# Performance work log

Measured on AMD Instinct MI355X. Metric: run time of the kernel, lower is better.

Reference implementation:

```python
import jax, jax.numpy as jnp
import numpy as np

B, OBJ, INP, HID = 8, 128, 64, 256
D = 3 * INP  # concatenated per-object feature dim


def setup_inputs() -> dict:
    key = jax.random.key(0)
    ks = jax.random.split(key, 12)
    s = 0.02
    return {
        "x0": jax.random.normal(ks[0], (B, OBJ, INP), jnp.float32),
        "x1": jax.random.normal(ks[1], (B, OBJ, INP), jnp.float32),
        "x2": jax.random.normal(ks[2], (B, OBJ, INP), jnp.float32),
        # weights stored [in, out] so forward is x @ w + b
        "w_enc": jax.random.normal(ks[3], (2 * D, HID), jnp.float32) * s,
        "b_enc": jnp.zeros((HID,), jnp.float32),
        "w1": jax.random.normal(ks[4], (HID, HID), jnp.float32) * s,
        "b1": jnp.zeros((HID,), jnp.float32),
        "w2": jax.random.normal(ks[5], (HID, HID), jnp.float32) * s,
        "b2": jnp.zeros((HID,), jnp.float32),
        "w3": jax.random.normal(ks[6], (HID, HID), jnp.float32) * s,
        "b3": jnp.zeros((HID,), jnp.float32),
        "wd1": jax.random.normal(ks[7], (HID, HID), jnp.float32) * s,
        "bd1": jnp.zeros((HID,), jnp.float32),
        "wd2": jax.random.normal(ks[8], (HID, INP), jnp.float32) * s,
        "bd2": jnp.zeros((INP,), jnp.float32),
    }


def reference(x0, x1, x2, w_enc, b_enc, w1, b1, w2, b2, w3, b3, wd1, bd1, wd2, bd2):
    x = jnp.concatenate([x0, x1, x2], axis=-1)  # [B, N, D]
    # Fused equivalent of Linear(cat(e1, e2)): split w_enc rows into the part
    # acting on the first-object features and the second-object features, then
    # broadcast-add instead of materializing the [B,N,N,2D] concat tensor.
    ea = jnp.einsum("bnd,dh->bnh", x, w_enc[:D])   # acts on data_e1
    eb = jnp.einsum("bnd,dh->bnh", x, w_enc[D:])   # acts on data_e2
    h = jax.nn.relu(ea[:, :, None, :] + eb[:, None, :, :] + b_enc)  # [B,N,N,H]
    h = jax.nn.relu(h @ w1 + b1)
    h = jax.nn.relu(h @ w2 + b2)
    h = h @ w3 + b3              # fc3 has no activation before the mean
    pooled = h.mean(axis=2)      # [B, N, H]
    out = jax.nn.relu(pooled @ wd1 + bd1) @ wd2 + bd2  # [B, N, INP]
    return out
```

## Files before the change

kernel.cpp:

```cpp
#include <hip/hip_runtime.h>
#include <stdint.h>


#define HID 256
#define NOBJ 128
#define NROW 1024

typedef __attribute__((ext_vector_type(8))) short short8;
typedef __attribute__((ext_vector_type(4))) float float4v;
typedef __attribute__((ext_vector_type(16))) float float16v;
typedef __attribute__((ext_vector_type(2))) unsigned int uint2v;

__device__ __forceinline__ unsigned int f2bf_u(float f) {
    unsigned int u = __builtin_bit_cast(unsigned int, f);
    u += 0x7fffu + ((u >> 16) & 1u);
    return u >> 16;
}
__device__ __forceinline__ unsigned int pack2(float a, float b) {
    return f2bf_u(a) | (f2bf_u(b) << 16);
}
__device__ __forceinline__ float relu(float v) { return v > 0.f ? v : 0.f; }

__device__ __forceinline__ void lds_barrier() {
    asm volatile("s_waitcnt lgkmcnt(0)\n\ts_barrier" ::: "memory");
}

__global__ void setup_kernel(const float* __restrict__ x0, const float* __restrict__ x1,
                             const float* __restrict__ x2, const float* __restrict__ w_enc,
                             const float* __restrict__ b_enc,
                             const float* __restrict__ w1, const float* __restrict__ w2,
                             const float* __restrict__ w3,
                             unsigned short* __restrict__ wt,
                             float* __restrict__ ea, float* __restrict__ eb) {
    const int bx = blockIdx.x, t = threadIdx.x;
    __shared__ float lw[256][33];
    __shared__ float xs[2][192];
    if (bx < 24) {
        const int m = bx >> 3, tau = bx & 7;
        const float* w = (m == 0) ? w1 : (m == 1) ? w2 : w3;
        const int n = t & 31, kk = t >> 5;
#pragma unroll
        for (int rep = 0; rep < 32; ++rep) {
            int k = rep * 8 + kk;
            lw[k][n] = w[k * 256 + tau * 32 + n];
        }
        __syncthreads();
        unsigned short* outp = wt + (m * 8 + tau) * 8192;
        const int lane = t & 63, wq = t >> 6;
        const int h5 = lane >> 5, l31n = lane & 31;
#pragma unroll
        for (int rep = 0; rep < 4; ++rep) {
            const int kb = wq * 4 + rep;
            short8 v;
#pragma unroll
            for (int e = 0; e < 8; ++e)
                v[e] = (short)f2bf_u(lw[kb * 16 + h5 * 8 + e][l31n]);
            *(short8*)(outp + kb * 512 + lane * 8) = v;
        }
        return;
    }
    const int e = bx - 24;
    for (int idx = t; idx < 384; idx += 256) {
        int r = idx / 192, d = idx % 192;
        int row = e * 2 + r;
        float v = (d < 64) ? x0[row * 64 + d]
                : (d < 128) ? x1[row * 64 + d - 64]
                : x2[row * 64 + d - 128];
        xs[r][d] = v;
    }
    __syncthreads();
    float aA[2] = {0.f, 0.f}, aB[2] = {0.f, 0.f};
#pragma unroll 16
    for (int d = 0; d < 192; ++d) {
        float wa = w_enc[d * 256 + t];
        float wb = w_enc[(192 + d) * 256 + t];
#pragma unroll
        for (int r = 0; r < 2; ++r) { aA[r] += xs[r][d] * wa; aB[r] += xs[r][d] * wb; }
    }
    float be = b_enc[t];
#pragma unroll
    for (int r = 0; r < 2; ++r) {
        ea[(e * 2 + r) * 256 + t] = aA[r] + be;
        eb[(e * 2 + r) * 256 + t] = aB[r];
    }
}

__global__ __launch_bounds__(256, 2) void pair_kernel(
        const float* __restrict__ ea, const float* __restrict__ eb,
        const unsigned short* __restrict__ wt,
        const float* __restrict__ b1, const float* __restrict__ b2,
        const float* __restrict__ b3,
        const float* __restrict__ wd1, const float* __restrict__ bd1,
        const float* __restrict__ wd2, const float* __restrict__ bd2,
        float* __restrict__ out) {
    __shared__ __align__(16) unsigned short hbuf[128 * 256];

    const int w = blockIdx.x, b = w >> 7;
    const int t = threadIdx.x, wv = t >> 6, lane = t & 63;
    const int l31 = lane & 31, h5 = lane >> 5;
    const int n0 = wv * 64;

    const unsigned short* aptr = wt + lane * 8;

    short8 af[4][2], bfr[2][4];
#pragma unroll
    for (int pg = 0; pg < 3; ++pg) {
        af[pg][0] = *(const short8*)(aptr + ((wv * 2 + 0) * 16 + pg) * 512);
        af[pg][1] = *(const short8*)(aptr + ((wv * 2 + 1) * 16 + pg) * 512);
    }

    {
        const float4v va = *(const float4v*)(ea + w * 256 + lane * 4);
        const float* ebbase = eb + (b * NOBJ) * 256;
        const int c = lane >> 1, sub = (lane & 1) * 4;
#pragma unroll 4
        for (int jj = 0; jj < 32; ++jj) {
            const int j = wv * 32 + jj;
            float4v vb = *(const float4v*)(ebbase + j * 256 + lane * 4);
            int addr = j * 256 + ((c ^ (j & 31)) << 3) + sub;
            *(uint2v*)(hbuf + addr) = (uint2v){
                pack2(relu(va[0] + vb[0]), relu(va[1] + vb[1])),
                pack2(relu(va[2] + vb[2]), relu(va[3] + vb[3]))};
        }
    }
    lds_barrier();

    int jb[4];
#pragma unroll
    for (int tj = 0; tj < 4; ++tj) jb[tj] = (tj * 32 + l31) * 256;
#pragma unroll
    for (int tj = 0; tj < 4; ++tj)
        bfr[0][tj] = *(const short8*)(hbuf + jb[tj] + ((h5 ^ l31) << 3));

    float16v acc[2][4];

#pragma unroll
    for (int l = 0; l < 3; ++l) {
        const float* bias = (l == 0) ? b1 : (l == 1) ? b2 : b3;
#pragma unroll
        for (int tn = 0; tn < 2; ++tn)
#pragma unroll
            for (int q = 0; q < 4; ++q) {
                float4v bv = *(const float4v*)(bias + n0 + tn * 32 + q * 8 + h5 * 4);
#pragma unroll
                for (int i = 0; i < 4; ++i)
#pragma unroll
                    for (int tj = 0; tj < 4; ++tj)
                        acc[tn][tj][q * 4 + i] = bv[i];
            }
#pragma unroll
        for (int kb = 0; kb < 16; ++kb) {
            const int g = l * 16 + kb, gp = g + 3;
            if (gp < 48) {
                const int lp = gp >> 4, kp = gp & 15;
                af[gp & 3][0] = *(const short8*)(aptr + ((lp * 8 + wv * 2 + 0) * 16 + kp) * 512);
                af[gp & 3][1] = *(const short8*)(aptr + ((lp * 8 + wv * 2 + 1) * 16 + kp) * 512);
            }
            if (kb < 15) {
                const int off = ((((kb + 1) * 2 + h5) ^ l31) << 3);
#pragma unroll
                for (int tj = 0; tj < 4; ++tj)
                    bfr[(kb + 1) & 1][tj] = *(const short8*)(hbuf + jb[tj] + off);
            }
#pragma unroll
            for (int tn = 0; tn < 2; ++tn)
#pragma unroll
                for (int tj = 0; tj < 4; ++tj)
                    acc[tn][tj] = __builtin_amdgcn_mfma_f32_32x32x16_bf16(
                        af[g & 3][tn], bfr[kb & 1][tj], acc[tn][tj], 0, 0, 0);
        }
        lds_barrier();

        if (l < 2) {
#pragma unroll
            for (int tn = 0; tn < 2; ++tn)
#pragma unroll
                for (int q = 0; q < 4; ++q) {
                    const int nb_ = n0 + tn * 32 + 8 * q + 4 * h5;
                    const int cn = nb_ >> 3, sub = nb_ & 7;
#pragma unroll
                    for (int tj = 0; tj < 4; ++tj) {
                        const int j = tj * 32 + l31;
                        int addr = j * 256 + ((cn ^ l31) << 3) + sub;
                        *(uint2v*)(hbuf + addr) = (uint2v){
                            pack2(relu(acc[tn][tj][q * 4]), relu(acc[tn][tj][q * 4 + 1])),
                            pack2(relu(acc[tn][tj][q * 4 + 2]), relu(acc[tn][tj][q * 4 + 3]))};
                    }
                }
            lds_barrier();
#pragma unroll
            for (int tj = 0; tj < 4; ++tj)
                bfr[0][tj] = *(const short8*)(hbuf + jb[tj] + ((h5 ^ l31) << 3));
        }
    }

    float* fs = (float*)hbuf;
    {
#pragma unroll
        for (int tn = 0; tn < 2; ++tn)
#pragma unroll
            for (int r = 0; r < 16; ++r) {
                float s = acc[tn][0][r] + acc[tn][1][r] + acc[tn][2][r] + acc[tn][3][r];
                s += __shfl_xor(s, 1);
                s += __shfl_xor(s, 2);
                s += __shfl_xor(s, 4);
                s += __shfl_xor(s, 8);
                s += __shfl_xor(s, 16);
                if (l31 == 0) {
                    const int n = n0 + tn * 32 + (r & 3) + 8 * (r >> 2) + 4 * h5;
                    fs[n] = s * 0.0078125f;
                }
            }
    }
    __syncthreads();
    {
        float a1 = bd1[t];
#pragma unroll 16
        for (int k = 0; k < 256; ++k) a1 += fs[k] * wd1[k * 256 + t];
        __syncthreads();
        fs[256 + t] = relu(a1);
    }
    __syncthreads();
    {
        const int o = lane;
        float p = 0.f;
        const float* w2p = wd2 + (wv * 64) * 64 + o;
#pragma unroll 16
        for (int kk = 0; kk < 64; ++kk) p += fs[256 + wv * 64 + kk] * w2p[kk * 64];
        fs[512 + wv * 64 + o] = p;
    }
    __syncthreads();
    if (t < 64)
        out[w * 64 + t] = fs[512 + t] + fs[576 + t] + fs[640 + t] + fs[704 + t] + bd2[t];
}

extern "C" void kernel_launch(void* const* d_in, const int* in_sizes, int n_in,
                              void* d_out, int out_size, void* d_ws, size_t ws_size,
                              hipStream_t stream) {
    const float* x0    = (const float*)d_in[0];
    const float* x1    = (const float*)d_in[1];
    const float* x2    = (const float*)d_in[2];
    const float* w_enc = (const float*)d_in[3];
    const float* b_enc = (const float*)d_in[4];
    const float* w1    = (const float*)d_in[5];
    const float* b1    = (const float*)d_in[6];
    const float* w2    = (const float*)d_in[7];
    const float* b2    = (const float*)d_in[8];
    const float* w3    = (const float*)d_in[9];
    const float* b3    = (const float*)d_in[10];
    const float* wd1   = (const float*)d_in[11];
    const float* bd1   = (const float*)d_in[12];
    const float* wd2   = (const float*)d_in[13];
    const float* bd2   = (const float*)d_in[14];
    float* out = (float*)d_out;

    unsigned short* wt = (unsigned short*)d_ws;
    float* ea = (float*)((char*)d_ws + 3 * 65536 * sizeof(unsigned short));
    float* eb = ea + NROW * HID;

    setup_kernel<<<536, 256, 0, stream>>>(x0, x1, x2, w_enc, b_enc, w1, w2, w3, wt, ea, eb);
    pair_kernel<<<NROW, 256, 0, stream>>>(ea, eb, wt, b1, b2, b3,
                                          wd1, bd1, wd2, bd2, out);
}
```

Before: 169.7 us.

## Store activation tile in MFMA fragment-major LDS layout instead of XOR swizzle

```diff
diff --git a/kernel.cpp b/kernel.cpp
--- a/kernel.cpp
+++ b/kernel.cpp
@@ -10,6 +10,7 @@
 typedef __attribute__((ext_vector_type(4))) float float4v;
 typedef __attribute__((ext_vector_type(16))) float float16v;
 typedef __attribute__((ext_vector_type(2))) unsigned int uint2v;
+typedef __attribute__((ext_vector_type(4))) unsigned int uint4v;
 
 __device__ __forceinline__ unsigned int f2bf_u(float f) {
     unsigned int u = __builtin_bit_cast(unsigned int, f);
@@ -110,27 +111,38 @@
     }
 
     {
-        const float4v va = *(const float4v*)(ea + w * 256 + lane * 4);
         const float* ebbase = eb + (b * NOBJ) * 256;
-        const int c = lane >> 1, sub = (lane & 1) * 4;
-#pragma unroll 4
-        for (int jj = 0; jj < 32; ++jj) {
-            const int j = wv * 32 + jj;
-            float4v vb = *(const float4v*)(ebbase + j * 256 + lane * 4);
-            int addr = j * 256 + ((c ^ (j & 31)) << 3) + sub;
-            *(uint2v*)(hbuf + addr) = (uint2v){
-                pack2(relu(va[0] + vb[0]), relu(va[1] + vb[1])),
-                pack2(relu(va[2] + vb[2]), relu(va[3] + vb[3]))};
+        const float* eap = ea + w * 256;
+        float4v ael[4][2];
+#pragma unroll
+        for (int kbl = 0; kbl < 4; ++kbl) {
+            const int k0 = (wv * 4 + kbl) * 16 + h5 * 8;
+            ael[kbl][0] = *(const float4v*)(eap + k0);
+            ael[kbl][1] = *(const float4v*)(eap + k0 + 4);
+        }
+#pragma unroll
+        for (int jl = 0; jl < 4; ++jl) {
+            const int j = jl * 32 + l31;
+#pragma unroll
+            for (int kbl = 0; kbl < 4; ++kbl) {
+                const int kb = wv * 4 + kbl;
+                const int k0 = kb * 16 + h5 * 8;
+                float4v e0 = *(const float4v*)(ebbase + j * 256 + k0);
+                float4v e1 = *(const float4v*)(ebbase + j * 256 + k0 + 4);
+                uint4v v;
+                v[0] = pack2(relu(ael[kbl][0][0] + e0[0]), relu(ael[kbl][0][1] + e0[1]));
+                v[1] = pack2(relu(ael[kbl][0][2] + e0[2]), relu(ael[kbl][0][3] + e0[3]));
+                v[2] = pack2(relu(ael[kbl][1][0] + e1[0]), relu(ael[kbl][1][1] + e1[1]));
+                v[3] = pack2(relu(ael[kbl][1][2] + e1[2]), relu(ael[kbl][1][3] + e1[3]));
+                *(uint4v*)(hbuf + (jl * 16 + kb) * 512 + lane * 8) = v;
+            }
         }
     }
     lds_barrier();
 
-    int jb[4];
-#pragma unroll
-    for (int tj = 0; tj < 4; ++tj) jb[tj] = (tj * 32 + l31) * 256;
 #pragma unroll
     for (int tj = 0; tj < 4; ++tj)
-        bfr[0][tj] = *(const short8*)(hbuf + jb[tj] + ((h5 ^ l31) << 3));
+        bfr[0][tj] = *(const short8*)(hbuf + (tj * 16) * 512 + lane * 8);
 
     float16v acc[2][4];
 
@@ -157,10 +169,10 @@
                 af[gp & 3][1] = *(const short8*)(aptr + ((lp * 8 + wv * 2 + 1) * 16 + kp) * 512);
             }
             if (kb < 15) {
-                const int off = ((((kb + 1) * 2 + h5) ^ l31) << 3);
 #pragma unroll
                 for (int tj = 0; tj < 4; ++tj)
-                    bfr[(kb + 1) & 1][tj] = *(const short8*)(hbuf + jb[tj] + off);
+                    bfr[(kb + 1) & 1][tj] =
+                        *(const short8*)(hbuf + (tj * 16 + kb + 1) * 512 + lane * 8);
             }
 #pragma unroll
             for (int tn = 0; tn < 2; ++tn)
@@ -177,11 +189,12 @@
 #pragma unroll
                 for (int q = 0; q < 4; ++q) {
                     const int nb_ = n0 + tn * 32 + 8 * q + 4 * h5;
-                    const int cn = nb_ >> 3, sub = nb_ & 7;
+                    const int kbf = nb_ >> 4;
+                    const int halfsel = (nb_ >> 3) & 1;
+                    const int sub = nb_ & 7;
 #pragma unroll
                     for (int tj = 0; tj < 4; ++tj) {
-                        const int j = tj * 32 + l31;
-                        int addr = j * 256 + ((cn ^ l31) << 3) + sub;
+                        int addr = (tj * 16 + kbf) * 512 + (halfsel * 32 + l31) * 8 + sub;
                         *(uint2v*)(hbuf + addr) = (uint2v){
                             pack2(relu(acc[tn][tj][q * 4]), relu(acc[tn][tj][q * 4 + 1])),
                             pack2(relu(acc[tn][tj][q * 4 + 2]), relu(acc[tn][tj][q * 4 + 3]))};
@@ -190,7 +203,7 @@
             lds_barrier();
 #pragma unroll
             for (int tj = 0; tj < 4; ++tj)
-                bfr[0][tj] = *(const short8*)(hbuf + jb[tj] + ((h5 ^ l31) << 3));
+                bfr[0][tj] = *(const short8*)(hbuf + (tj * 16) * 512 + lane * 8);
         }
     }
 
```

Result: slower. 174.9 us (+3.1%).
